# Optimization experiments

Hardware: AMD Instinct MI355X
Metric: run time of the kernel (lower is better)

## Reference

```python
import jax, jax.numpy as jnp
import numpy as np

B, NODES, D, DEG = 256, 124, 32, 16
N = B * NODES
EP = NODES * DEG
E = B * EP
L, H, C = 3, 4, 32
NCLS = 40
TMP = 124 + 32 * 2 * L
EPS = 1e-5
NEG_SLOPE = 0.2


def setup_inputs() -> dict:
    key = jax.random.key(0)
    ks = jax.random.split(key, 16)
    x = jax.random.normal(ks[0], (N, D), dtype=jnp.float32)
    # per-graph random edges, guaranteed no self-loops
    src = jax.random.randint(ks[1], (B, EP), 0, NODES)
    off = jax.random.randint(ks[2], (B, EP), 1, NODES)
    dst = (src + off) % NODES
    goff = (jnp.arange(B) * NODES)[:, None]
    edge_index = jnp.stack([(src + goff).reshape(-1), (dst + goff).reshape(-1)]).astype(jnp.int32)
    batch = jnp.repeat(jnp.arange(B), NODES).astype(jnp.int32)
    conv_W = jax.random.normal(ks[3], (L, D, H * C), dtype=jnp.float32) / np.sqrt(D)
    conv_att_l = jax.random.normal(ks[4], (L, H, C), dtype=jnp.float32) * 0.1
    conv_att_r = jax.random.normal(ks[5], (L, H, C), dtype=jnp.float32) * 0.1
    conv_bias = jnp.zeros((L, C), dtype=jnp.float32)
    bn_gamma = jnp.ones((L, C), dtype=jnp.float32)
    bn_beta = jnp.zeros((L, C), dtype=jnp.float32)
    lin1_W = jax.random.normal(ks[6], (NODES * C, 124), dtype=jnp.float32) / np.sqrt(NODES * C)
    lin1_b = jnp.zeros((124,), dtype=jnp.float32)
    bn1_gamma = jnp.ones((124,), dtype=jnp.float32)
    bn1_beta = jnp.zeros((124,), dtype=jnp.float32)
    lin2_W = jax.random.normal(ks[7], (TMP, NCLS), dtype=jnp.float32) / np.sqrt(TMP)
    lin2_b = jnp.zeros((NCLS,), dtype=jnp.float32)
    return dict(x=x, edge_index=edge_index, batch=batch, conv_W=conv_W,
                conv_att_l=conv_att_l, conv_att_r=conv_att_r, conv_bias=conv_bias,
                bn_gamma=bn_gamma, bn_beta=bn_beta, lin1_W=lin1_W, lin1_b=lin1_b,
                bn1_gamma=bn1_gamma, bn1_beta=bn1_beta, lin2_W=lin2_W, lin2_b=lin2_b)


def _supergat_mx(x, src, dst, W, att_l, att_r, bias):
    # SuperGATConv, attention_type='MX', concat=False (mean over heads), eval mode
    h = (x @ W).reshape(N, H, C)              # [N,H,C]
    x_j = h[src]                              # source / message features [E',H,C]
    x_i = h[dst]                              # target features
    logits = jnp.sum(x_i * x_j, -1)           # [E',H] dot-product logits
    alpha = jnp.sum(x_j * att_l, -1) + jnp.sum(x_i * att_r, -1)
    alpha = alpha * jax.nn.sigmoid(logits)
    alpha = jax.nn.leaky_relu(alpha, NEG_SLOPE)
    # scatter-softmax over incoming edges of each target node
    amax = jax.ops.segment_max(alpha, dst, num_segments=N)
    ex = jnp.exp(alpha - amax[dst])
    denom = jax.ops.segment_sum(ex, dst, num_segments=N)
    a = ex / (denom[dst] + 1e-16)             # [E',H]
    out = jax.ops.segment_sum(x_j * a[..., None], dst, num_segments=N)  # [N,H,C]
    return out.mean(axis=1) + bias            # concat=False -> head mean, [N,C]


def _batchnorm(x, gamma, beta):
    mu = x.mean(0)
    var = x.var(0)
    return (x - mu) * jax.lax.rsqrt(var + EPS) * gamma + beta


def reference(x, edge_index, batch, conv_W, conv_att_l, conv_att_r, conv_bias,
              bn_gamma, bn_beta, lin1_W, lin1_b, bn1_gamma, bn1_beta, lin2_W, lin2_b):
    # add self loops once (input edges contain none)
    sl = jnp.arange(N, dtype=edge_index.dtype)
    src = jnp.concatenate([edge_index[0], sl])
    dst = jnp.concatenate([edge_index[1], sl])
    inter = []
    for l in range(L):
        x = _supergat_mx(x, src, dst, conv_W[l], conv_att_l[l], conv_att_r[l], conv_bias[l])
        x = _batchnorm(x, bn_gamma[l], bn_beta[l])
        x = jax.nn.relu(x)
        cnt = jax.ops.segment_sum(jnp.ones((N,), x.dtype), batch, num_segments=B)
        gmean = jax.ops.segment_sum(x, batch, num_segments=B) / cnt[:, None]
        gmax = jax.ops.segment_max(x, batch, num_segments=B)
        inter.append(jnp.concatenate([gmean, gmax], 1))   # [B, 2C]
    x = x.reshape(B, NODES * C)
    x = x @ lin1_W + lin1_b
    x = _batchnorm(x, bn1_gamma, bn1_beta)
    x = jnp.concatenate([x] + inter, 1)                   # inter_connect=True
    x = jax.nn.relu(x)
    return x @ lin2_W + lin2_b                            # [B, NCLS]
```

## Files before the change

### kernel.cpp

```cpp
#include <hip/hip_runtime.h>
#include <math.h>

#define NN 31744
#define NE 507904
#define EP 1984
#define NODES 124
#define NB 256
#define CC 32
#define HC 128
#define FEAT_DIM 316
#define NCLS 40
#define NC 3968
#define EXCAP 192

typedef __attribute__((ext_vector_type(8))) short bf16x8;
typedef __attribute__((ext_vector_type(4))) float f32x4;

#define LOG2E  1.44269504f
#define LOG2E5 0.28853901f

__device__ __forceinline__ unsigned short f2bf(float f) {
    unsigned u = __float_as_uint(f);
    u = u + 0x7FFFu + ((u >> 16) & 1u);
    return (unsigned short)(u >> 16);
}
__device__ __forceinline__ float bf2f(unsigned short s) {
    return __uint_as_float(((unsigned)s) << 16);
}

__global__ __launch_bounds__(256) void mask_build(const int* __restrict__ ei,
                                                  unsigned* __restrict__ gmask,
                                                  int* __restrict__ gdst,
                                                  int* __restrict__ gdent,
                                                  float* __restrict__ bnacc) {
    __shared__ unsigned mcnt[NODES * NODES];
    __shared__ int cnt[128], pref[128];
    __shared__ int locs[124][8];
    int g = blockIdx.x, t = threadIdx.x;
    if (g == 0 && t < 192) bnacc[t] = 0.f;
    for (int i = t; i < NODES * NODES; i += 256) mcnt[i] = 0u;
    __syncthreads();
    for (int e = t; e < EP; e += 256) {
        int s = ei[g * EP + e] - g * NODES;
        int d = ei[NE + g * EP + e] - g * NODES;
        atomicAdd(&mcnt[d * NODES + s], 1u);
    }
    __syncthreads();
    int nd = 0;
    if (t < 124) {
        unsigned m[4] = {0u, 0u, 0u, 0u};
        for (int s = 0; s < NODES; ++s) {
            unsigned c = mcnt[t * NODES + s] + (s == t ? 1u : 0u);
            if (c) {
                m[s >> 5] |= 1u << (s & 31);
                if (c > 1u && nd < 8) { locs[t][nd] = (s << 8) | (int)c; nd++; }
            }
        }
        uint4 mm; mm.x = m[0]; mm.y = m[1]; mm.z = m[2]; mm.w = m[3];
        *(uint4*)&gmask[(size_t)(g * NODES + t) * 4] = mm;
        cnt[t] = nd;
    } else if (t < 128) cnt[t] = 0;
    __syncthreads();
    if (t < 128) pref[t] = cnt[t];
    __syncthreads();
    for (int off = 1; off < 128; off <<= 1) {
        int v = (t >= off && t < 128) ? pref[t - off] : 0;
        __syncthreads();
        if (t < 128) pref[t] += v;
        __syncthreads();
    }
    if (t < 124) {
        int off = pref[t] - cnt[t];
        gdst[g * 132 + t] = off < EXCAP ? off : EXCAP;
        for (int j = 0; j < nd; ++j)
            if (off + j < EXCAP) gdent[g * EXCAP + off + j] = locs[t][j];
    }
    if (t == 0) {
        int tot = pref[127];
        gdst[g * 132 + 124] = tot < EXCAP ? tot : EXCAP;
    }
}

__global__ __launch_bounds__(256) void wtrans(const float* __restrict__ W,
                                              unsigned short* __restrict__ WT) {
    __shared__ float tile[32][33];
    int kb = blockIdx.x, jb = blockIdx.y;
    int t = threadIdx.x;
    int tr = t >> 5, tc = t & 31;
    for (int r = tr; r < 32; r += 8) {
        int k = kb * 32 + r, j = jb * 32 + tc;
        tile[r][tc] = (j < 124) ? W[k * 124 + j] : 0.f;
    }
    __syncthreads();
    for (int r = tr; r < 32; r += 8) {
        int j = jb * 32 + r, k = kb * 32 + tc;
        WT[(size_t)j * NC + k] = f2bf(tile[tc][r]);
    }
}

#define HS 136
#define TS 136
#define XS 40
#define ABS 136
#define PWS 40

__global__ __launch_bounds__(1024, 1) void conv_graph(
    const float* __restrict__ xin, const float* __restrict__ W,
    const float* __restrict__ attl, const float* __restrict__ attr,
    const float* __restrict__ bias,
    const unsigned* __restrict__ gmask, const int* __restrict__ gdst,
    const int* __restrict__ gdent,
    const float* __restrict__ bnprev, const float* __restrict__ gprev,
    const float* __restrict__ bprev, float* __restrict__ feat, int lprev,
    float* __restrict__ y, float* __restrict__ bnacc) {

    __shared__ short hbh[128 * HS];
    __shared__ short hbl[128 * HS];
    __shared__ short hTall[128 * TS];
    __shared__ short pwbuf[16 * 1280];
    __shared__ short attBuf[16 * ABS];
    __shared__ float ALs[4][128], ARs[4][128];
    __shared__ unsigned mask[128][4];
    __shared__ unsigned short dupst[136];
    __shared__ unsigned dupent[EXCAP];
    __shared__ float bias_s[32];
    __shared__ float bsum[8][32], bsq[8][32];
    __shared__ float pmean[32];
    __shared__ int pmax[32];

    int g = blockIdx.x, t = threadIdx.x, base = g * NODES;
    short* xh  = pwbuf;
    short* xl  = pwbuf + 5120;
    short* WTh = hTall;
    short* WTl = hTall + 5120;

    if (t < 32) { pmean[t] = 0.f; pmax[t] = 0; }
    __syncthreads();

    {
        const float4* xsrc = (const float4*)(xin + (size_t)base * CC);
        for (int i = t; i < 992; i += 1024) {
            float4 v = xsrc[i];
            int n = i >> 3, c4 = i & 7;
            if (lprev >= 0) {
                float vv[4] = {v.x, v.y, v.z, v.w};
#pragma unroll
                for (int q = 0; q < 4; ++q) {
                    int c = c4 * 4 + q;
                    float mu = bnprev[c] * (1.f / NN);
                    float var = bnprev[32 + c] * (1.f / NN) - mu * mu;
                    float sc = rsqrtf(var + 1e-5f) * gprev[c];
                    float xv = (vv[q] - mu) * sc + bprev[c];
                    xv = fmaxf(xv, 0.f);
                    vv[q] = xv;
                    atomicAdd(&pmean[c], xv);
                    atomicMax(&pmax[c], __float_as_int(xv));
                }
                v.x = vv[0]; v.y = vv[1]; v.z = vv[2]; v.w = vv[3];
            }
            unsigned short h0 = f2bf(v.x), h1 = f2bf(v.y), h2 = f2bf(v.z), h3 = f2bf(v.w);
            unsigned short l0 = f2bf(v.x - bf2f(h0)), l1 = f2bf(v.y - bf2f(h1));
            unsigned short l2 = f2bf(v.z - bf2f(h2)), l3 = f2bf(v.w - bf2f(h3));
            uint2 ph; ph.x = ((unsigned)h1 << 16) | h0; ph.y = ((unsigned)h3 << 16) | h2;
            uint2 pl; pl.x = ((unsigned)l1 << 16) | l0; pl.y = ((unsigned)l3 << 16) | l2;
            *(uint2*)&xh[n * XS + c4 * 4] = ph;
            *(uint2*)&xl[n * XS + c4 * 4] = pl;
        }
        if (t < 4 * XS) { xh[124 * XS + t] = 0; xl[124 * XS + t] = 0; }
    }
    {
        int hc = t & 127, mq = t >> 7, ks = mq * 4;
        unsigned short hh4[4], ll4[4];
#pragma unroll
        for (int q = 0; q < 4; ++q) {
            float w = W[(ks + q) * HC + hc];
            hh4[q] = f2bf(w);
            ll4[q] = f2bf(w - bf2f(hh4[q]));
        }
        uint2 ph; ph.x = ((unsigned)hh4[1] << 16) | hh4[0]; ph.y = ((unsigned)hh4[3] << 16) | hh4[2];
        uint2 pl; pl.x = ((unsigned)ll4[1] << 16) | ll4[0]; pl.y = ((unsigned)ll4[3] << 16) | ll4[2];
        *(uint2*)&WTh[hc * XS + ks] = ph;
        *(uint2*)&WTl[hc * XS + ks] = pl;
    }
    for (int i = t; i < 2048; i += 1024) {
        int n = i >> 7, k = i & 127;
        float v = 0.f;
        int hidx = n & 3;
        if (n < 8 && (k >> 5) == hidx)
            v = (n < 4) ? attl[hidx * 32 + (k & 31)] : attr[hidx * 32 + (k & 31)];
        attBuf[n * ABS + k] = (short)f2bf(v);
    }
    if (t < CC) bias_s[t] = bias[t];
    if (t < 128) {
        if (t < 124) {
            uint4 m = *(const uint4*)&gmask[(size_t)(base + t) * 4];
            mask[t][0] = m.x; mask[t][1] = m.y; mask[t][2] = m.z; mask[t][3] = m.w;
        } else { mask[t][0] = 0u; mask[t][1] = 0u; mask[t][2] = 0u; mask[t][3] = 0u; }
    }
    if (t < 136) dupst[t] = (unsigned short)gdst[g * 132 + (t < 124 ? t : 124)];
    if (t >= 832 && t < 832 + EXCAP) dupent[t - 832] = (unsigned)gdent[g * EXCAP + (t - 832)];
    __syncthreads();

    if (lprev >= 0 && t < 32) {
        float* fp = feat + g * FEAT_DIM + NODES + lprev * 64;
        fp[t] = pmean[t] * (1.f / NODES);
        fp[32 + t] = __int_as_float(pmax[t]);
    }

    int wv = t >> 6, l = t & 63;
    int l15 = l & 15, l4 = l >> 4;

#pragma unroll
    for (int j = 0; j < 4; ++j) {
        int idx = wv * 4 + j;
        int tr = idx >> 3, tc = idx & 7;
        bf16x8 ah = *(bf16x8*)&xh[(tr * 16 + l15) * XS + l4 * 8];
        bf16x8 al_ = *(bf16x8*)&xl[(tr * 16 + l15) * XS + l4 * 8];
        bf16x8 bh = *(bf16x8*)&WTh[(tc * 16 + l15) * XS + l4 * 8];
        bf16x8 bl_ = *(bf16x8*)&WTl[(tc * 16 + l15) * XS + l4 * 8];
        f32x4 z = {0.f, 0.f, 0.f, 0.f};
        f32x4 c0 = __builtin_amdgcn_mfma_f32_16x16x32_bf16(ah, bh, z, 0, 0, 0);
        f32x4 c1 = __builtin_amdgcn_mfma_f32_16x16x32_bf16(ah, bl_, z, 0, 0, 0);
        f32x4 c2 = __builtin_amdgcn_mfma_f32_16x16x32_bf16(al_, bh, z, 0, 0, 0);
        f32x4 c = (c0 + c1) + c2;
        int hc = tc * 16 + l15;
#pragma unroll
        for (int r = 0; r < 4; ++r) {
            int n = tr * 16 + l4 * 4 + r;
            float s = c[r];
            unsigned short hi = f2bf(s);
            hbh[n * HS + hc] = (short)hi;
            hbl[n * HS + hc] = (short)f2bf(s - bf2f(hi));
        }
    }
    __syncthreads();

    if (wv < 8) {
        f32x4 c = {0.f, 0.f, 0.f, 0.f};
#pragma unroll
        for (int kb = 0; kb < 4; ++kb) {
            bf16x8 a = *(bf16x8*)&hbh[(wv * 16 + l15) * HS + kb * 32 + l4 * 8];
            bf16x8 b = *(bf16x8*)&attBuf[l15 * ABS + kb * 32 + l4 * 8];
            c = __builtin_amdgcn_mfma_f32_16x16x32_bf16(a, b, c, 0, 0, 0);
        }
        if (l15 < 8) {
#pragma unroll
            for (int r = 0; r < 4; ++r) {
                int n = wv * 16 + l4 * 4 + r;
                if (l15 < 4) ALs[l15][n] = c[r];
                else         ARs[l15 - 4][n] = c[r];
            }
        }
    }
#pragma unroll
    for (int hh2 = 0; hh2 < 4; ++hh2) {
        int k = t & 31, n4 = t >> 5;
        unsigned short r4[4];
#pragma unroll
        for (int r = 0; r < 4; ++r)
            r4[r] = (unsigned short)hbh[(n4 * 4 + r) * HS + hh2 * 32 + k];
        uint2 pk;
        pk.x = ((unsigned)r4[1] << 16) | r4[0];
        pk.y = ((unsigned)r4[3] << 16) | r4[2];
        *(uint2*)&hTall[(hh2 * 32 + k) * TS + n4 * 4] = pk;
    }
    __syncthreads();

    int DJ = wv >> 1;
    float accA[4] = {0.f, 0.f, 0.f, 0.f};
    float accB[4] = {0.f, 0.f, 0.f, 0.f};
    {
        int hh0 = (wv & 1) * 2;
        short* pwb = pwbuf + wv * 1280;
        int dst = DJ * 16 + l15;
        uint4 mrow = *(uint4*)&mask[dst][0];
        unsigned mwords[4] = {mrow.x, mrow.y, mrow.z, mrow.w};
        unsigned cntp[8];
#pragma unroll
        for (int SI = 0; SI < 8; ++SI) {
            unsigned mw = (mwords[SI >> 1] >> ((SI & 1) * 16 + l4 * 4)) & 0xFu;
            cntp[SI] = (mw & 1u) | ((mw & 2u) << 7) | ((mw & 4u) << 14) | ((mw & 8u) << 21);
        }
        {
            int s0 = dupst[dst], s1 = dupst[dst + 1];
            for (int e = s0; e < s1; ++e) {
                unsigned ent = dupent[e];
                unsigned src = (ent >> 8) & 255u;
                unsigned SI = src >> 4;
                unsigned r = (src & 15u) - (unsigned)(l4 * 4);
                if (r < 4u) {
                    unsigned sh = 8u * r;
                    cntp[SI] = (cntp[SI] & ~(255u << sh)) | ((ent & 255u) << sh);
                }
            }
        }

#define GRAM(kb, slot) { \
    _Pragma("unroll") \
    for (int s2 = 0; s2 < 2; ++s2) { \
        int SI = (kb) * 2 + s2; \
        int ao = (SI * 16 + l15) * HS + hh * 32 + l4 * 8; \
        bf16x8 ah = *(bf16x8*)&hbh[ao]; \
        bf16x8 al_ = *(bf16x8*)&hbl[ao]; \
        f32x4 z2 = {0.f, 0.f, 0.f, 0.f}; \
        f32x4 c0 = __builtin_amdgcn_mfma_f32_16x16x32_bf16(ah, gb, z2, 0, 0, 0); \
        f32x4 c1 = __builtin_amdgcn_mfma_f32_16x16x32_bf16(ah, gl, z2, 0, 0, 0); \
        f32x4 c2 = __builtin_amdgcn_mfma_f32_16x16x32_bf16(al_, gb, z2, 0, 0, 0); \
        f32x4 c = (c0 + c1) + c2; \
        int src0 = SI * 16 + l4 * 4; \
        float4 al4 = *(float4*)&ALs[hh][src0]; \
        unsigned cp = cntp[SI]; \
        float pv[4]; \
        _Pragma("unroll") \
        for (int r = 0; r < 4; ++r) { \
            float e2 = __builtin_amdgcn_exp2f(-LOG2E * c[r]); \
            float sig = __builtin_amdgcn_rcpf(1.f + e2); \
            float a2 = (((const float*)&al4)[r] + ar) * sig; \
            float m = fmaxf(a2 * LOG2E, a2 * LOG2E5); \
            float cr = (float)((cp >> (8 * r)) & 255u); \
            pv[r] = __builtin_amdgcn_exp2f(m) * cr; \
        } \
        sden += (pv[0] + pv[1]) + (pv[2] + pv[3]); \
        unsigned w0_, w1_; \
        asm("v_cvt_pk_bf16_f32 %0, %1, %2" : "=v"(w0_) : "v"(pv[0]), "v"(pv[1])); \
        asm("v_cvt_pk_bf16_f32 %0, %1, %2" : "=v"(w1_) : "v"(pv[2]), "v"(pv[3])); \
        uint2 pk_; pk_.x = w0_; pk_.y = w1_; \
        *(uint2*)&pwb[(slot) * 640 + l15 * PWS + s2 * 16 + l4 * 4] = pk_; \
    } }

#define PVOP(kb, slot) { \
    bf16x8 a = *(bf16x8*)&pwb[(slot) * 640 + l15 * PWS + l4 * 8]; \
    bf16x8 b0 = *(bf16x8*)&hTall[(hh * 32 + l15) * TS + (kb) * 32 + l4 * 8]; \
    bf16x8 b1 = *(bf16x8*)&hTall[(hh * 32 + 16 + l15) * TS + (kb) * 32 + l4 * 8]; \
    num0 = __builtin_amdgcn_mfma_f32_16x16x32_bf16(a, b0, num0, 0, 0, 0); \
    num1 = __builtin_amdgcn_mfma_f32_16x16x32_bf16(a, b1, num1, 0, 0, 0); }

#pragma unroll
        for (int jj = 0; jj < 2; ++jj) {
            int hh = hh0 + jj;
            bf16x8 gb = *(bf16x8*)&hbh[dst * HS + hh * 32 + l4 * 8];
            bf16x8 gl = *(bf16x8*)&hbl[dst * HS + hh * 32 + l4 * 8];
            float ar = ARs[hh][dst];
            float sden = 0.f;
            f32x4 num0 = {0.f, 0.f, 0.f, 0.f};
            f32x4 num1 = {0.f, 0.f, 0.f, 0.f};
            GRAM(0, 0);
            GRAM(1, 1); PVOP(0, 0);
            GRAM(2, 0); PVOP(1, 1);
            GRAM(3, 1); PVOP(2, 0);
            PVOP(3, 1);
            sden += __shfl_xor(sden, 16, 64);
            sden += __shfl_xor(sden, 32, 64);
#pragma unroll
            for (int r = 0; r < 4; ++r) {
                float dn = __shfl(sden, l4 * 4 + r, 64) + 1e-16f;
                accA[r] += ((float*)&num0)[r] / dn;
                accB[r] += ((float*)&num1)[r] / dn;
            }
        }
#undef GRAM
#undef PVOP
    }
    __syncthreads();

    float* exch = (float*)pwbuf;
    if (wv & 1) {
#pragma unroll
        for (int r = 0; r < 4; ++r) {
            exch[DJ * 512 + l15 * 16 + l4 * 4 + r] = accA[r];
            exch[DJ * 512 + 256 + l15 * 16 + l4 * 4 + r] = accB[r];
        }
    }
    __syncthreads();

    if (!(wv & 1)) {
        float sA = 0.f, qA = 0.f, sB = 0.f, qB = 0.f;
#pragma unroll
        for (int r = 0; r < 4; ++r) {
            int n = DJ * 16 + l4 * 4 + r;
            float a = accA[r] + exch[DJ * 512 + l15 * 16 + l4 * 4 + r];
            float b = accB[r] + exch[DJ * 512 + 256 + l15 * 16 + l4 * 4 + r];
            a = 0.25f * a + bias_s[l15];
            b = 0.25f * b + bias_s[16 + l15];
            if (n < NODES) {
                y[(size_t)(base + n) * CC + l15] = a;
                y[(size_t)(base + n) * CC + 16 + l15] = b;
                sA += a; qA += a * a; sB += b; qB += b * b;
            }
        }
        sA += __shfl_xor(sA, 16, 64); sA += __shfl_xor(sA, 32, 64);
        qA += __shfl_xor(qA, 16, 64); qA += __shfl_xor(qA, 32, 64);
        sB += __shfl_xor(sB, 16, 64); sB += __shfl_xor(sB, 32, 64);
        qB += __shfl_xor(qB, 16, 64); qB += __shfl_xor(qB, 32, 64);
        if (l < 16) {
            bsum[DJ][l15] = sA; bsum[DJ][16 + l15] = sB;
            bsq[DJ][l15] = qA;  bsq[DJ][16 + l15] = qB;
        }
    }
    __syncthreads();
    if (t < CC) {
        float S = 0.f, Q = 0.f;
#pragma unroll
        for (int w = 0; w < 8; ++w) { S += bsum[w][t]; Q += bsq[w][t]; }
        atomicAdd(&bnacc[t], S);
        atomicAdd(&bnacc[CC + t], Q);
    }
}

__global__ void bn_relu_pool(const float* __restrict__ y, const float* __restrict__ acc,
                             const float* __restrict__ gamma, const float* __restrict__ beta,
                             unsigned short* __restrict__ xbf, float* __restrict__ feat, int l) {
    int g = blockIdx.x;
    int t = threadIdx.x;
    int c = t & 31, r0 = t >> 5;
    float mu = acc[c] * (1.f / NN);
    float var = acc[32 + c] * (1.f / NN) - mu * mu;
    float sc = rsqrtf(var + 1e-5f) * gamma[c];
    float bt = beta[c];
    float s = 0.f, mx = -INFINITY;
    for (int r = r0; r < NODES; r += 4) {
        int i = (g * NODES + r) * CC + c;
        float v = (y[i] - mu) * sc + bt;
        v = fmaxf(v, 0.f);
        xbf[i] = f2bf(v);
        s += v; mx = fmaxf(mx, v);
    }
    __shared__ float ls[128], lm[128];
    ls[t] = s; lm[t] = mx;
    __syncthreads();
    if (t < 32) {
        float S = ls[t] + ls[32 + t] + ls[64 + t] + ls[96 + t];
        float M = fmaxf(fmaxf(lm[t], lm[32 + t]), fmaxf(lm[64 + t], lm[96 + t]));
        float* fp = feat + g * FEAT_DIM + NODES + l * 64;
        fp[t] = S * (1.f / NODES);
        fp[32 + t] = M;
    }
}

#define L1_KS 4
#define L1_KC 992
#define XP 1000
__global__ __launch_bounds__(512) void lin1_mfma(const unsigned short* __restrict__ Xb,
                                                 const unsigned short* __restrict__ WT,
                                                 float* __restrict__ part) {
    __shared__ unsigned short Xs[16 * XP];
    int mt = blockIdx.x >> 2, kp = blockIdx.x & 3;
    int t = threadIdx.x;
    int wv = t >> 6, l = t & 63, l15 = l & 15, l4 = l >> 4;
    int M0 = mt * 16, k0 = kp * L1_KC;
    for (int i = t; i < 16 * 124; i += 512) {
        int r = i / 124, c = i - r * 124;
        *(uint4*)&Xs[r * XP + c * 8] = *(const uint4*)&Xb[(size_t)(M0 + r) * NC + k0 + c * 8];
    }
    __syncthreads();
    int N0 = wv * 16;
    f32x4 acc = {0.f, 0.f, 0.f, 0.f};
#pragma unroll 4
    for (int kk = 0; kk < 31; ++kk) {
        bf16x8 a = *(bf16x8*)&Xs[l15 * XP + kk * 32 + l4 * 8];
        bf16x8 b = *(const bf16x8*)&WT[(size_t)(N0 + l15) * NC + k0 + kk * 32 + l4 * 8];
        acc = __builtin_amdgcn_mfma_f32_16x16x32_bf16(a, b, acc, 0, 0, 0);
    }
    if (N0 + l15 < 124) {
#pragma unroll
        for (int r = 0; r < 4; ++r)
            part[(size_t)kp * NB * 124 + (M0 + l4 * 4 + r) * 124 + N0 + l15] = acc[r];
    }
}

__global__ void lin1_reduce(const float* __restrict__ part, const float* __restrict__ b,
                            float* __restrict__ out1) {
    int i = blockIdx.x * blockDim.x + threadIdx.x;
    if (i >= NB * 124) return;
    int j = i % 124;
    float s = b[j];
#pragma unroll
    for (int ks = 0; ks < L1_KS; ++ks) s += part[ks * NB * 124 + i];
    out1[i] = s;
}

__global__ void bn1_relu(const float* __restrict__ out1, const float* __restrict__ gamma,
                         const float* __restrict__ beta, float* __restrict__ feat) {
    __shared__ float ps[4][124], pq[4][124], smu[124], ssc[124], sbt[124];
    int t = threadIdx.x;
    int c = t & 127, seg = t >> 7;
    float s = 0.f, q = 0.f;
    if (c < 124) {
        for (int b = seg * 64; b < seg * 64 + 64; ++b) {
            float v = out1[b * 124 + c]; s += v; q += v * v;
        }
        ps[seg][c] = s; pq[seg][c] = q;
    }
    __syncthreads();
    if (t < 124) {
        float S = ps[0][t] + ps[1][t] + ps[2][t] + ps[3][t];
        float Q = pq[0][t] + pq[1][t] + pq[2][t] + pq[3][t];
        float mu = S * (1.f / NB);
        float var = Q * (1.f / NB) - mu * mu;
        smu[t] = mu; ssc[t] = rsqrtf(var + 1e-5f) * gamma[t]; sbt[t] = beta[t];
    }
    __syncthreads();
    if (c < 124) {
        for (int b = seg * 64; b < seg * 64 + 64; ++b) {
            float v = (out1[b * 124 + c] - smu[c]) * ssc[c] + sbt[c];
            feat[b * FEAT_DIM + c] = fmaxf(v, 0.f);
        }
    }
}

__global__ void lin2_k(const float* __restrict__ feat, const float* __restrict__ W,
                       const float* __restrict__ b, float* __restrict__ out) {
    __shared__ float psum[8][40];
    int g = blockIdx.x;
    int t = threadIdx.x;
    int j = t % 40, u = t / 40;
    if (u < 8) {
        int k0 = u * 40, k1 = (u == 7) ? FEAT_DIM : k0 + 40;
        float s = 0.f;
        for (int k = k0; k < k1; ++k) s += feat[g * FEAT_DIM + k] * W[k * NCLS + j];
        psum[u][j] = s;
    }
    __syncthreads();
    if (t < NCLS) {
        float s = b[t];
#pragma unroll
        for (int u2 = 0; u2 < 8; ++u2) s += psum[u2][t];
        out[g * NCLS + t] = s;
    }
}

extern "C" void kernel_launch(void* const* d_in, const int* in_sizes, int n_in,
                              void* d_out, int out_size, void* d_ws, size_t ws_size,
                              hipStream_t stream) {
    const float* x      = (const float*)d_in[0];
    const int*   ei     = (const int*)d_in[1];
    const float* conv_W = (const float*)d_in[3];
    const float* att_l  = (const float*)d_in[4];
    const float* att_r  = (const float*)d_in[5];
    const float* conv_b = (const float*)d_in[6];
    const float* bn_g   = (const float*)d_in[7];
    const float* bn_b   = (const float*)d_in[8];
    const float* lin1_W = (const float*)d_in[9];
    const float* lin1_b = (const float*)d_in[10];
    const float* bn1_g  = (const float*)d_in[11];
    const float* bn1_b  = (const float*)d_in[12];
    const float* lin2_W = (const float*)d_in[13];
    const float* lin2_b = (const float*)d_in[14];

    float* ws = (float*)d_ws;
    float* y = ws;
    unsigned short* xbf = (unsigned short*)(y + (size_t)NN * CC);
    float* bnacc = (float*)(xbf + (size_t)NN * CC);
    float* feat  = bnacc + 192;
    float* out1  = feat + NB * FEAT_DIM;
    float* part  = out1 + NB * 124;
    unsigned short* WT = (unsigned short*)(part + L1_KS * NB * 124);
    unsigned* gmask = (unsigned*)(WT + (size_t)128 * NC);
    int* gdst  = (int*)(gmask + (size_t)NN * 4);
    int* gdent = gdst + NB * 132;

    mask_build<<<NB, 256, 0, stream>>>(ei, gmask, gdst, gdent, bnacc);
    wtrans<<<dim3(NC / 32, 4), 256, 0, stream>>>(lin1_W, WT);

    const float* xin = x;
    for (int l = 0; l < 3; ++l) {
        const float* bnprev = (l == 0) ? nullptr : bnacc + (l - 1) * 64;
        const float* gprev  = (l == 0) ? bn_g : bn_g + (l - 1) * CC;
        const float* bprev  = (l == 0) ? bn_b : bn_b + (l - 1) * CC;
        conv_graph<<<NB, 1024, 0, stream>>>(xin, conv_W + l * CC * HC,
                                            att_l + l * HC, att_r + l * HC,
                                            conv_b + l * CC, gmask, gdst, gdent,
                                            bnprev, gprev, bprev, feat, l - 1,
                                            y, bnacc + l * 64);
        xin = y;
    }

    bn_relu_pool<<<NB, 128, 0, stream>>>(y, bnacc + 128, bn_g + 2 * CC, bn_b + 2 * CC,
                                         xbf, feat, 2);
    lin1_mfma<<<64, 512, 0, stream>>>(xbf, WT, part);
    lin1_reduce<<<(NB * 124 + 255) / 256, 256, 0, stream>>>(part, lin1_b, out1);
    bn1_relu<<<1, 512, 0, stream>>>(out1, bn1_g, bn1_b, feat);
    lin2_k<<<NB, 320, 0, stream>>>(feat, lin2_W, lin2_b, (float*)d_out);
}
```

Before: 145.6 us.

## Fuse mask build, three conv layers and BN pooling into one cooperative kernel

```diff
diff --git a/kernel.cpp b/kernel.cpp
--- a/kernel.cpp
+++ b/kernel.cpp
@@ -1,5 +1,8 @@
 #include <hip/hip_runtime.h>
+#include <hip/hip_cooperative_groups.h>
 #include <math.h>
+
+namespace cg = cooperative_groups;
 
 #define NN 31744
 #define NE 507904
@@ -28,64 +31,13 @@
     return __uint_as_float(((unsigned)s) << 16);
 }
 
-__global__ __launch_bounds__(256) void mask_build(const int* __restrict__ ei,
-                                                  unsigned* __restrict__ gmask,
-                                                  int* __restrict__ gdst,
-                                                  int* __restrict__ gdent,
-                                                  float* __restrict__ bnacc) {
-    __shared__ unsigned mcnt[NODES * NODES];
-    __shared__ int cnt[128], pref[128];
-    __shared__ int locs[124][8];
-    int g = blockIdx.x, t = threadIdx.x;
-    if (g == 0 && t < 192) bnacc[t] = 0.f;
-    for (int i = t; i < NODES * NODES; i += 256) mcnt[i] = 0u;
-    __syncthreads();
-    for (int e = t; e < EP; e += 256) {
-        int s = ei[g * EP + e] - g * NODES;
-        int d = ei[NE + g * EP + e] - g * NODES;
-        atomicAdd(&mcnt[d * NODES + s], 1u);
-    }
-    __syncthreads();
-    int nd = 0;
-    if (t < 124) {
-        unsigned m[4] = {0u, 0u, 0u, 0u};
-        for (int s = 0; s < NODES; ++s) {
-            unsigned c = mcnt[t * NODES + s] + (s == t ? 1u : 0u);
-            if (c) {
-                m[s >> 5] |= 1u << (s & 31);
-                if (c > 1u && nd < 8) { locs[t][nd] = (s << 8) | (int)c; nd++; }
-            }
-        }
-        uint4 mm; mm.x = m[0]; mm.y = m[1]; mm.z = m[2]; mm.w = m[3];
-        *(uint4*)&gmask[(size_t)(g * NODES + t) * 4] = mm;
-        cnt[t] = nd;
-    } else if (t < 128) cnt[t] = 0;
-    __syncthreads();
-    if (t < 128) pref[t] = cnt[t];
-    __syncthreads();
-    for (int off = 1; off < 128; off <<= 1) {
-        int v = (t >= off && t < 128) ? pref[t - off] : 0;
-        __syncthreads();
-        if (t < 128) pref[t] += v;
-        __syncthreads();
-    }
-    if (t < 124) {
-        int off = pref[t] - cnt[t];
-        gdst[g * 132 + t] = off < EXCAP ? off : EXCAP;
-        for (int j = 0; j < nd; ++j)
-            if (off + j < EXCAP) gdent[g * EXCAP + off + j] = locs[t][j];
-    }
-    if (t == 0) {
-        int tot = pref[127];
-        gdst[g * 132 + 124] = tot < EXCAP ? tot : EXCAP;
-    }
-}
-
 __global__ __launch_bounds__(256) void wtrans(const float* __restrict__ W,
-                                              unsigned short* __restrict__ WT) {
+                                              unsigned short* __restrict__ WT,
+                                              float* __restrict__ bnacc) {
     __shared__ float tile[32][33];
     int kb = blockIdx.x, jb = blockIdx.y;
     int t = threadIdx.x;
+    if (kb == 0 && jb == 0 && t < 192) bnacc[t] = 0.f;
     int tr = t >> 5, tc = t & 31;
     for (int r = tr; r < 32; r += 8) {
         int k = kb * 32 + r, j = jb * 32 + tc;
@@ -104,18 +56,15 @@
 #define ABS 136
 #define PWS 40
 
-__global__ __launch_bounds__(1024, 1) void conv_graph(
-    const float* __restrict__ xin, const float* __restrict__ W,
+__global__ __launch_bounds__(1024, 1) void conv3(
+    const float* __restrict__ x, const float* __restrict__ Wall,
     const float* __restrict__ attl, const float* __restrict__ attr,
-    const float* __restrict__ bias,
-    const unsigned* __restrict__ gmask, const int* __restrict__ gdst,
-    const int* __restrict__ gdent,
-    const float* __restrict__ bnprev, const float* __restrict__ gprev,
-    const float* __restrict__ bprev, float* __restrict__ feat, int lprev,
-    float* __restrict__ y, float* __restrict__ bnacc) {
-
-    __shared__ short hbh[128 * HS];
-    __shared__ short hbl[128 * HS];
+    const float* __restrict__ ball, const float* __restrict__ bng,
+    const float* __restrict__ bnb, const int* __restrict__ ei,
+    unsigned short* __restrict__ xbf, float* __restrict__ feat,
+    float* __restrict__ bnacc) {
+
+    __shared__ short hpool[2 * 128 * HS];
     __shared__ short hTall[128 * TS];
     __shared__ short pwbuf[16 * 1280];
     __shared__ short attBuf[16 * ABS];
@@ -125,175 +74,196 @@
     __shared__ unsigned dupent[EXCAP];
     __shared__ float bias_s[32];
     __shared__ float bsum[8][32], bsq[8][32];
-    __shared__ float pmean[32];
-    __shared__ int pmax[32];
-
-    int g = blockIdx.x, t = threadIdx.x, base = g * NODES;
+    __shared__ int cnt_s[128], pref_s[128];
+
+    short* hbh = hpool;
+    short* hbl = hpool + 128 * HS;
     short* xh  = pwbuf;
     short* xl  = pwbuf + 5120;
     short* WTh = hTall;
     short* WTl = hTall + 5120;
 
-    if (t < 32) { pmean[t] = 0.f; pmax[t] = 0; }
-    __syncthreads();
+    cg::grid_group grid = cg::this_grid();
+    int g = blockIdx.x, t = threadIdx.x, base = g * NODES;
+    int wv = t >> 6, l = t & 63;
+    int l15 = l & 15, l4 = l >> 4;
+    int DJ = wv >> 1;
 
     {
-        const float4* xsrc = (const float4*)(xin + (size_t)base * CC);
-        for (int i = t; i < 992; i += 1024) {
-            float4 v = xsrc[i];
-            int n = i >> 3, c4 = i & 7;
-            if (lprev >= 0) {
-                float vv[4] = {v.x, v.y, v.z, v.w};
-#pragma unroll
-                for (int q = 0; q < 4; ++q) {
-                    int c = c4 * 4 + q;
-                    float mu = bnprev[c] * (1.f / NN);
-                    float var = bnprev[32 + c] * (1.f / NN) - mu * mu;
-                    float sc = rsqrtf(var + 1e-5f) * gprev[c];
-                    float xv = (vv[q] - mu) * sc + bprev[c];
-                    xv = fmaxf(xv, 0.f);
-                    vv[q] = xv;
-                    atomicAdd(&pmean[c], xv);
-                    atomicMax(&pmax[c], __float_as_int(xv));
-                }
-                v.x = vv[0]; v.y = vv[1]; v.z = vv[2]; v.w = vv[3];
-            }
+        const float4* xsrc = (const float4*)(x + (size_t)base * CC);
+        if (t < 992) {
+            float4 v = xsrc[t];
+            int n = t >> 3, c4 = t & 7;
             unsigned short h0 = f2bf(v.x), h1 = f2bf(v.y), h2 = f2bf(v.z), h3 = f2bf(v.w);
-            unsigned short l0 = f2bf(v.x - bf2f(h0)), l1 = f2bf(v.y - bf2f(h1));
-            unsigned short l2 = f2bf(v.z - bf2f(h2)), l3 = f2bf(v.w - bf2f(h3));
+            unsigned short q0 = f2bf(v.x - bf2f(h0)), q1 = f2bf(v.y - bf2f(h1));
+            unsigned short q2 = f2bf(v.z - bf2f(h2)), q3 = f2bf(v.w - bf2f(h3));
             uint2 ph; ph.x = ((unsigned)h1 << 16) | h0; ph.y = ((unsigned)h3 << 16) | h2;
-            uint2 pl; pl.x = ((unsigned)l1 << 16) | l0; pl.y = ((unsigned)l3 << 16) | l2;
+            uint2 pl; pl.x = ((unsigned)q1 << 16) | q0; pl.y = ((unsigned)q3 << 16) | q2;
             *(uint2*)&xh[n * XS + c4 * 4] = ph;
             *(uint2*)&xl[n * XS + c4 * 4] = pl;
         }
         if (t < 4 * XS) { xh[124 * XS + t] = 0; xl[124 * XS + t] = 0; }
     }
+
     {
-        int hc = t & 127, mq = t >> 7, ks = mq * 4;
-        unsigned short hh4[4], ll4[4];
-#pragma unroll
-        for (int q = 0; q < 4; ++q) {
-            float w = W[(ks + q) * HC + hc];
-            hh4[q] = f2bf(w);
-            ll4[q] = f2bf(w - bf2f(hh4[q]));
-        }
-        uint2 ph; ph.x = ((unsigned)hh4[1] << 16) | hh4[0]; ph.y = ((unsigned)hh4[3] << 16) | hh4[2];
-        uint2 pl; pl.x = ((unsigned)ll4[1] << 16) | ll4[0]; pl.y = ((unsigned)ll4[3] << 16) | ll4[2];
-        *(uint2*)&WTh[hc * XS + ks] = ph;
-        *(uint2*)&WTl[hc * XS + ks] = pl;
-    }
-    for (int i = t; i < 2048; i += 1024) {
-        int n = i >> 7, k = i & 127;
-        float v = 0.f;
-        int hidx = n & 3;
-        if (n < 8 && (k >> 5) == hidx)
-            v = (n < 4) ? attl[hidx * 32 + (k & 31)] : attr[hidx * 32 + (k & 31)];
-        attBuf[n * ABS + k] = (short)f2bf(v);
-    }
-    if (t < CC) bias_s[t] = bias[t];
-    if (t < 128) {
+        unsigned* mcnt = (unsigned*)hpool;
+        int (*locs)[8] = (int(*)[8])hTall;
+        for (int i = t; i < NODES * NODES; i += 1024) mcnt[i] = 0u;
+        __syncthreads();
+        for (int e = t; e < EP; e += 1024) {
+            int s = ei[g * EP + e] - base;
+            int d = ei[NE + g * EP + e] - base;
+            atomicAdd(&mcnt[d * NODES + s], 1u);
+        }
+        __syncthreads();
+        int nd = 0;
         if (t < 124) {
-            uint4 m = *(const uint4*)&gmask[(size_t)(base + t) * 4];
-            mask[t][0] = m.x; mask[t][1] = m.y; mask[t][2] = m.z; mask[t][3] = m.w;
-        } else { mask[t][0] = 0u; mask[t][1] = 0u; mask[t][2] = 0u; mask[t][3] = 0u; }
-    }
-    if (t < 136) dupst[t] = (unsigned short)gdst[g * 132 + (t < 124 ? t : 124)];
-    if (t >= 832 && t < 832 + EXCAP) dupent[t - 832] = (unsigned)gdent[g * EXCAP + (t - 832)];
-    __syncthreads();
-
-    if (lprev >= 0 && t < 32) {
-        float* fp = feat + g * FEAT_DIM + NODES + lprev * 64;
-        fp[t] = pmean[t] * (1.f / NODES);
-        fp[32 + t] = __int_as_float(pmax[t]);
-    }
-
-    int wv = t >> 6, l = t & 63;
-    int l15 = l & 15, l4 = l >> 4;
-
-#pragma unroll
-    for (int j = 0; j < 4; ++j) {
-        int idx = wv * 4 + j;
-        int tr = idx >> 3, tc = idx & 7;
-        bf16x8 ah = *(bf16x8*)&xh[(tr * 16 + l15) * XS + l4 * 8];
-        bf16x8 al_ = *(bf16x8*)&xl[(tr * 16 + l15) * XS + l4 * 8];
-        bf16x8 bh = *(bf16x8*)&WTh[(tc * 16 + l15) * XS + l4 * 8];
-        bf16x8 bl_ = *(bf16x8*)&WTl[(tc * 16 + l15) * XS + l4 * 8];
-        f32x4 z = {0.f, 0.f, 0.f, 0.f};
-        f32x4 c0 = __builtin_amdgcn_mfma_f32_16x16x32_bf16(ah, bh, z, 0, 0, 0);
-        f32x4 c1 = __builtin_amdgcn_mfma_f32_16x16x32_bf16(ah, bl_, z, 0, 0, 0);
-        f32x4 c2 = __builtin_amdgcn_mfma_f32_16x16x32_bf16(al_, bh, z, 0, 0, 0);
-        f32x4 c = (c0 + c1) + c2;
-        int hc = tc * 16 + l15;
-#pragma unroll
-        for (int r = 0; r < 4; ++r) {
-            int n = tr * 16 + l4 * 4 + r;
-            float s = c[r];
-            unsigned short hi = f2bf(s);
-            hbh[n * HS + hc] = (short)hi;
-            hbl[n * HS + hc] = (short)f2bf(s - bf2f(hi));
-        }
-    }
-    __syncthreads();
-
-    if (wv < 8) {
-        f32x4 c = {0.f, 0.f, 0.f, 0.f};
-#pragma unroll
-        for (int kb = 0; kb < 4; ++kb) {
-            bf16x8 a = *(bf16x8*)&hbh[(wv * 16 + l15) * HS + kb * 32 + l4 * 8];
-            bf16x8 b = *(bf16x8*)&attBuf[l15 * ABS + kb * 32 + l4 * 8];
-            c = __builtin_amdgcn_mfma_f32_16x16x32_bf16(a, b, c, 0, 0, 0);
-        }
-        if (l15 < 8) {
+            unsigned m[4] = {0u, 0u, 0u, 0u};
+            for (int s = 0; s < NODES; ++s) {
+                unsigned c = mcnt[t * NODES + s] + (s == t ? 1u : 0u);
+                if (c) {
+                    m[s >> 5] |= 1u << (s & 31);
+                    if (c > 1u && nd < 8) { locs[t][nd] = (s << 8) | (int)c; nd++; }
+                }
+            }
+            mask[t][0] = m[0]; mask[t][1] = m[1]; mask[t][2] = m[2]; mask[t][3] = m[3];
+            cnt_s[t] = nd;
+        } else if (t < 128) {
+            cnt_s[t] = 0;
+            mask[t][0] = 0u; mask[t][1] = 0u; mask[t][2] = 0u; mask[t][3] = 0u;
+        }
+        __syncthreads();
+        if (t < 128) pref_s[t] = cnt_s[t];
+        __syncthreads();
+        for (int off = 1; off < 128; off <<= 1) {
+            int v = (t >= off && t < 128) ? pref_s[t - off] : 0;
+            __syncthreads();
+            if (t < 128) pref_s[t] += v;
+            __syncthreads();
+        }
+        if (t < 124) {
+            int off = pref_s[t] - cnt_s[t];
+            dupst[t] = (unsigned short)(off < EXCAP ? off : EXCAP);
+            for (int j = 0; j < nd; ++j)
+                if (off + j < EXCAP) dupent[off + j] = (unsigned)locs[t][j];
+        } else if (t < 136) {
+            int tot = pref_s[127];
+            dupst[t] = (unsigned short)(tot < EXCAP ? tot : EXCAP);
+        }
+        __syncthreads();
+    }
+
+    for (int lyr = 0; lyr < 3; ++lyr) {
+        const float* W = Wall + lyr * CC * HC;
+        {
+            int hc = t & 127, mq = t >> 7, ks = mq * 4;
+            unsigned short hh4[4], ll4[4];
+#pragma unroll
+            for (int q = 0; q < 4; ++q) {
+                float w = W[(ks + q) * HC + hc];
+                hh4[q] = f2bf(w);
+                ll4[q] = f2bf(w - bf2f(hh4[q]));
+            }
+            uint2 ph; ph.x = ((unsigned)hh4[1] << 16) | hh4[0]; ph.y = ((unsigned)hh4[3] << 16) | hh4[2];
+            uint2 pl; pl.x = ((unsigned)ll4[1] << 16) | ll4[0]; pl.y = ((unsigned)ll4[3] << 16) | ll4[2];
+            *(uint2*)&WTh[hc * XS + ks] = ph;
+            *(uint2*)&WTl[hc * XS + ks] = pl;
+        }
+        for (int i = t; i < 2048; i += 1024) {
+            int n = i >> 7, k = i & 127;
+            float v = 0.f;
+            int hidx = n & 3;
+            if (n < 8 && (k >> 5) == hidx)
+                v = (n < 4) ? attl[lyr * HC + hidx * 32 + (k & 31)]
+                            : attr[lyr * HC + hidx * 32 + (k & 31)];
+            attBuf[n * ABS + k] = (short)f2bf(v);
+        }
+        if (t < CC) bias_s[t] = ball[lyr * CC + t];
+        __syncthreads();
+
+#pragma unroll
+        for (int j = 0; j < 4; ++j) {
+            int idx = wv * 4 + j;
+            int tr = idx >> 3, tc = idx & 7;
+            bf16x8 ah = *(bf16x8*)&xh[(tr * 16 + l15) * XS + l4 * 8];
+            bf16x8 al_ = *(bf16x8*)&xl[(tr * 16 + l15) * XS + l4 * 8];
+            bf16x8 bh = *(bf16x8*)&WTh[(tc * 16 + l15) * XS + l4 * 8];
+            bf16x8 bl_ = *(bf16x8*)&WTl[(tc * 16 + l15) * XS + l4 * 8];
+            f32x4 z = {0.f, 0.f, 0.f, 0.f};
+            f32x4 c0 = __builtin_amdgcn_mfma_f32_16x16x32_bf16(ah, bh, z, 0, 0, 0);
+            f32x4 c1 = __builtin_amdgcn_mfma_f32_16x16x32_bf16(ah, bl_, z, 0, 0, 0);
+            f32x4 c2 = __builtin_amdgcn_mfma_f32_16x16x32_bf16(al_, bh, z, 0, 0, 0);
+            f32x4 c = (c0 + c1) + c2;
+            int hc = tc * 16 + l15;
 #pragma unroll
             for (int r = 0; r < 4; ++r) {
-                int n = wv * 16 + l4 * 4 + r;
-                if (l15 < 4) ALs[l15][n] = c[r];
-                else         ARs[l15 - 4][n] = c[r];
-            }
-        }
-    }
-#pragma unroll
-    for (int hh2 = 0; hh2 < 4; ++hh2) {
-        int k = t & 31, n4 = t >> 5;
-        unsigned short r4[4];
-#pragma unroll
-        for (int r = 0; r < 4; ++r)
-            r4[r] = (unsigned short)hbh[(n4 * 4 + r) * HS + hh2 * 32 + k];
-        uint2 pk;
-        pk.x = ((unsigned)r4[1] << 16) | r4[0];
-        pk.y = ((unsigned)r4[3] << 16) | r4[2];
-        *(uint2*)&hTall[(hh2 * 32 + k) * TS + n4 * 4] = pk;
-    }
-    __syncthreads();
-
-    int DJ = wv >> 1;
-    float accA[4] = {0.f, 0.f, 0.f, 0.f};
-    float accB[4] = {0.f, 0.f, 0.f, 0.f};
-    {
-        int hh0 = (wv & 1) * 2;
-        short* pwb = pwbuf + wv * 1280;
-        int dst = DJ * 16 + l15;
-        uint4 mrow = *(uint4*)&mask[dst][0];
-        unsigned mwords[4] = {mrow.x, mrow.y, mrow.z, mrow.w};
-        unsigned cntp[8];
-#pragma unroll
-        for (int SI = 0; SI < 8; ++SI) {
-            unsigned mw = (mwords[SI >> 1] >> ((SI & 1) * 16 + l4 * 4)) & 0xFu;
-            cntp[SI] = (mw & 1u) | ((mw & 2u) << 7) | ((mw & 4u) << 14) | ((mw & 8u) << 21);
-        }
+                int n = tr * 16 + l4 * 4 + r;
+                float s = c[r];
+                unsigned short hi = f2bf(s);
+                hbh[n * HS + hc] = (short)hi;
+                hbl[n * HS + hc] = (short)f2bf(s - bf2f(hi));
+            }
+        }
+        __syncthreads();
+
+        if (wv < 8) {
+            f32x4 c = {0.f, 0.f, 0.f, 0.f};
+#pragma unroll
+            for (int kb = 0; kb < 4; ++kb) {
+                bf16x8 a = *(bf16x8*)&hbh[(wv * 16 + l15) * HS + kb * 32 + l4 * 8];
+                bf16x8 b = *(bf16x8*)&attBuf[l15 * ABS + kb * 32 + l4 * 8];
+                c = __builtin_amdgcn_mfma_f32_16x16x32_bf16(a, b, c, 0, 0, 0);
+            }
+            if (l15 < 8) {
+#pragma unroll
+                for (int r = 0; r < 4; ++r) {
+                    int n = wv * 16 + l4 * 4 + r;
+                    if (l15 < 4) ALs[l15][n] = c[r];
+                    else         ARs[l15 - 4][n] = c[r];
+                }
+            }
+        }
+#pragma unroll
+        for (int hh2 = 0; hh2 < 4; ++hh2) {
+            int k = t & 31, n4 = t >> 5;
+            unsigned short r4[4];
+#pragma unroll
+            for (int r = 0; r < 4; ++r)
+                r4[r] = (unsigned short)hbh[(n4 * 4 + r) * HS + hh2 * 32 + k];
+            uint2 pk;
+            pk.x = ((unsigned)r4[1] << 16) | r4[0];
+            pk.y = ((unsigned)r4[3] << 16) | r4[2];
+            *(uint2*)&hTall[(hh2 * 32 + k) * TS + n4 * 4] = pk;
+        }
+        __syncthreads();
+
+        float accA[4] = {0.f, 0.f, 0.f, 0.f};
+        float accB[4] = {0.f, 0.f, 0.f, 0.f};
         {
-            int s0 = dupst[dst], s1 = dupst[dst + 1];
-            for (int e = s0; e < s1; ++e) {
-                unsigned ent = dupent[e];
-                unsigned src = (ent >> 8) & 255u;
-                unsigned SI = src >> 4;
-                unsigned r = (src & 15u) - (unsigned)(l4 * 4);
-                if (r < 4u) {
-                    unsigned sh = 8u * r;
-                    cntp[SI] = (cntp[SI] & ~(255u << sh)) | ((ent & 255u) << sh);
+            int hh0 = (wv & 1) * 2;
+            short* pwb = pwbuf + wv * 1280;
+            int dst = DJ * 16 + l15;
+            uint4 mrow = *(uint4*)&mask[dst][0];
+            unsigned mwords[4] = {mrow.x, mrow.y, mrow.z, mrow.w};
+            unsigned cntp[8];
+#pragma unroll
+            for (int SI = 0; SI < 8; ++SI) {
+                unsigned mw = (mwords[SI >> 1] >> ((SI & 1) * 16 + l4 * 4)) & 0xFu;
+                cntp[SI] = (mw & 1u) | ((mw & 2u) << 7) | ((mw & 4u) << 14) | ((mw & 8u) << 21);
+            }
+            {
+                int s0 = dupst[dst], s1 = dupst[dst + 1];
+                for (int e = s0; e < s1; ++e) {
+                    unsigned ent = dupent[e];
+                    unsigned src = (ent >> 8) & 255u;
+                    unsigned SI = src >> 4;
+                    unsigned r = (src & 15u) - (unsigned)(l4 * 4);
+                    if (r < 4u) {
+                        unsigned sh = 8u * r;
+                        cntp[SI] = (cntp[SI] & ~(255u << sh)) | ((ent & 255u) << sh);
+                    }
                 }
             }
-        }
 
 #define GRAM(kb, slot) { \
     _Pragma("unroll") \
@@ -336,104 +306,126 @@
     num1 = __builtin_amdgcn_mfma_f32_16x16x32_bf16(a, b1, num1, 0, 0, 0); }
 
 #pragma unroll
-        for (int jj = 0; jj < 2; ++jj) {
-            int hh = hh0 + jj;
-            bf16x8 gb = *(bf16x8*)&hbh[dst * HS + hh * 32 + l4 * 8];
-            bf16x8 gl = *(bf16x8*)&hbl[dst * HS + hh * 32 + l4 * 8];
-            float ar = ARs[hh][dst];
-            float sden = 0.f;
-            f32x4 num0 = {0.f, 0.f, 0.f, 0.f};
-            f32x4 num1 = {0.f, 0.f, 0.f, 0.f};
-            GRAM(0, 0);
-            GRAM(1, 1); PVOP(0, 0);
-            GRAM(2, 0); PVOP(1, 1);
-            GRAM(3, 1); PVOP(2, 0);
-            PVOP(3, 1);
-            sden += __shfl_xor(sden, 16, 64);
-            sden += __shfl_xor(sden, 32, 64);
-#pragma unroll
-            for (int r = 0; r < 4; ++r) {
-                float dn = __shfl(sden, l4 * 4 + r, 64) + 1e-16f;
-                accA[r] += ((float*)&num0)[r] / dn;
-                accB[r] += ((float*)&num1)[r] / dn;
-            }
-        }
+            for (int jj = 0; jj < 2; ++jj) {
+                int hh = hh0 + jj;
+                bf16x8 gb = *(bf16x8*)&hbh[dst * HS + hh * 32 + l4 * 8];
+                bf16x8 gl = *(bf16x8*)&hbl[dst * HS + hh * 32 + l4 * 8];
+                float ar = ARs[hh][dst];
+                float sden = 0.f;
+                f32x4 num0 = {0.f, 0.f, 0.f, 0.f};
+                f32x4 num1 = {0.f, 0.f, 0.f, 0.f};
+                GRAM(0, 0);
+                GRAM(1, 1); PVOP(0, 0);
+                GRAM(2, 0); PVOP(1, 1);
+                GRAM(3, 1); PVOP(2, 0);
+                PVOP(3, 1);
+                sden += __shfl_xor(sden, 16, 64);
+                sden += __shfl_xor(sden, 32, 64);
+#pragma unroll
+                for (int r = 0; r < 4; ++r) {
+                    float dn = __shfl(sden, l4 * 4 + r, 64) + 1e-16f;
+                    accA[r] += ((float*)&num0)[r] / dn;
+                    accB[r] += ((float*)&num1)[r] / dn;
+                }
+            }
 #undef GRAM
 #undef PVOP
-    }
-    __syncthreads();
-
-    float* exch = (float*)pwbuf;
-    if (wv & 1) {
-#pragma unroll
-        for (int r = 0; r < 4; ++r) {
-            exch[DJ * 512 + l15 * 16 + l4 * 4 + r] = accA[r];
-            exch[DJ * 512 + 256 + l15 * 16 + l4 * 4 + r] = accB[r];
-        }
-    }
-    __syncthreads();
-
-    if (!(wv & 1)) {
-        float sA = 0.f, qA = 0.f, sB = 0.f, qB = 0.f;
-#pragma unroll
-        for (int r = 0; r < 4; ++r) {
-            int n = DJ * 16 + l4 * 4 + r;
-            float a = accA[r] + exch[DJ * 512 + l15 * 16 + l4 * 4 + r];
-            float b = accB[r] + exch[DJ * 512 + 256 + l15 * 16 + l4 * 4 + r];
-            a = 0.25f * a + bias_s[l15];
-            b = 0.25f * b + bias_s[16 + l15];
-            if (n < NODES) {
-                y[(size_t)(base + n) * CC + l15] = a;
-                y[(size_t)(base + n) * CC + 16 + l15] = b;
-                sA += a; qA += a * a; sB += b; qB += b * b;
-            }
-        }
-        sA += __shfl_xor(sA, 16, 64); sA += __shfl_xor(sA, 32, 64);
-        qA += __shfl_xor(qA, 16, 64); qA += __shfl_xor(qA, 32, 64);
-        sB += __shfl_xor(sB, 16, 64); sB += __shfl_xor(sB, 32, 64);
-        qB += __shfl_xor(qB, 16, 64); qB += __shfl_xor(qB, 32, 64);
-        if (l < 16) {
-            bsum[DJ][l15] = sA; bsum[DJ][16 + l15] = sB;
-            bsq[DJ][l15] = qA;  bsq[DJ][16 + l15] = qB;
-        }
-    }
-    __syncthreads();
-    if (t < CC) {
-        float S = 0.f, Q = 0.f;
-#pragma unroll
-        for (int w = 0; w < 8; ++w) { S += bsum[w][t]; Q += bsq[w][t]; }
-        atomicAdd(&bnacc[t], S);
-        atomicAdd(&bnacc[CC + t], Q);
-    }
-}
-
-__global__ void bn_relu_pool(const float* __restrict__ y, const float* __restrict__ acc,
-                             const float* __restrict__ gamma, const float* __restrict__ beta,
-                             unsigned short* __restrict__ xbf, float* __restrict__ feat, int l) {
-    int g = blockIdx.x;
-    int t = threadIdx.x;
-    int c = t & 31, r0 = t >> 5;
-    float mu = acc[c] * (1.f / NN);
-    float var = acc[32 + c] * (1.f / NN) - mu * mu;
-    float sc = rsqrtf(var + 1e-5f) * gamma[c];
-    float bt = beta[c];
-    float s = 0.f, mx = -INFINITY;
-    for (int r = r0; r < NODES; r += 4) {
-        int i = (g * NODES + r) * CC + c;
-        float v = (y[i] - mu) * sc + bt;
-        v = fmaxf(v, 0.f);
-        xbf[i] = f2bf(v);
-        s += v; mx = fmaxf(mx, v);
-    }
-    __shared__ float ls[128], lm[128];
-    ls[t] = s; lm[t] = mx;
-    __syncthreads();
-    if (t < 32) {
-        float S = ls[t] + ls[32 + t] + ls[64 + t] + ls[96 + t];
-        float M = fmaxf(fmaxf(lm[t], lm[32 + t]), fmaxf(lm[64 + t], lm[96 + t]));
-        float* fp = feat + g * FEAT_DIM + NODES + l * 64;
-        fp[t] = S * (1.f / NODES);
-        fp[32 + t] = M;
+        }
+        __syncthreads();
+
+        float* exch = (float*)pwbuf;
+        if (wv & 1) {
+#pragma unroll
+            for (int r = 0; r < 4; ++r) {
+                exch[DJ * 512 + l15 * 16 + l4 * 4 + r] = accA[r];
+                exch[DJ * 512 + 256 + l15 * 16 + l4 * 4 + r] = accB[r];
+            }
+        }
+        __syncthreads();
+
+        float va[4] = {0.f, 0.f, 0.f, 0.f};
+        float vb[4] = {0.f, 0.f, 0.f, 0.f};
+        if (!(wv & 1)) {
+            float sA = 0.f, qA = 0.f, sB = 0.f, qB = 0.f;
+#pragma unroll
+            for (int r = 0; r < 4; ++r) {
+                int n = DJ * 16 + l4 * 4 + r;
+                float a = accA[r] + exch[DJ * 512 + l15 * 16 + l4 * 4 + r];
+                float b = accB[r] + exch[DJ * 512 + 256 + l15 * 16 + l4 * 4 + r];
+                a = 0.25f * a + bias_s[l15];
+                b = 0.25f * b + bias_s[16 + l15];
+                va[r] = a; vb[r] = b;
+                if (n < NODES) { sA += a; qA += a * a; sB += b; qB += b * b; }
+            }
+            sA += __shfl_xor(sA, 16, 64); sA += __shfl_xor(sA, 32, 64);
+            qA += __shfl_xor(qA, 16, 64); qA += __shfl_xor(qA, 32, 64);
+            sB += __shfl_xor(sB, 16, 64); sB += __shfl_xor(sB, 32, 64);
+            qB += __shfl_xor(qB, 16, 64); qB += __shfl_xor(qB, 32, 64);
+            if (l < 16) {
+                bsum[DJ][l15] = sA; bsum[DJ][16 + l15] = sB;
+                bsq[DJ][l15] = qA;  bsq[DJ][16 + l15] = qB;
+            }
+        }
+        __syncthreads();
+        if (t < CC) {
+            float S = 0.f, Q = 0.f;
+#pragma unroll
+            for (int w = 0; w < 8; ++w) { S += bsum[w][t]; Q += bsq[w][t]; }
+            atomicAdd(&bnacc[lyr * 64 + t], S);
+            atomicAdd(&bnacc[lyr * 64 + CC + t], Q);
+        }
+        grid.sync();
+
+        if (!(wv & 1)) {
+            float muA = bnacc[lyr * 64 + l15] * (1.f / NN);
+            float vrA = bnacc[lyr * 64 + 32 + l15] * (1.f / NN) - muA * muA;
+            float scA = rsqrtf(vrA + 1e-5f) * bng[lyr * CC + l15];
+            float btA = bnb[lyr * CC + l15];
+            float muB = bnacc[lyr * 64 + 16 + l15] * (1.f / NN);
+            float vrB = bnacc[lyr * 64 + 48 + l15] * (1.f / NN) - muB * muB;
+            float scB = rsqrtf(vrB + 1e-5f) * bng[lyr * CC + 16 + l15];
+            float btB = bnb[lyr * CC + 16 + l15];
+            float sA = 0.f, mA = -INFINITY, sB = 0.f, mB = -INFINITY;
+#pragma unroll
+            for (int r = 0; r < 4; ++r) {
+                int n = DJ * 16 + l4 * 4 + r;
+                float a = fmaxf((va[r] - muA) * scA + btA, 0.f);
+                float b = fmaxf((vb[r] - muB) * scB + btB, 0.f);
+                if (n < NODES) {
+                    sA += a; mA = fmaxf(mA, a); sB += b; mB = fmaxf(mB, b);
+                    if (lyr < 2) {
+                        unsigned short ha = f2bf(a);
+                        xh[n * XS + l15] = (short)ha;
+                        xl[n * XS + l15] = (short)f2bf(a - bf2f(ha));
+                        unsigned short hb = f2bf(b);
+                        xh[n * XS + 16 + l15] = (short)hb;
+                        xl[n * XS + 16 + l15] = (short)f2bf(b - bf2f(hb));
+                    } else {
+                        xbf[(size_t)(base + n) * CC + l15] = f2bf(a);
+                        xbf[(size_t)(base + n) * CC + 16 + l15] = f2bf(b);
+                    }
+                }
+            }
+            sA += __shfl_xor(sA, 16, 64); sA += __shfl_xor(sA, 32, 64);
+            sB += __shfl_xor(sB, 16, 64); sB += __shfl_xor(sB, 32, 64);
+            mA = fmaxf(mA, __shfl_xor(mA, 16, 64)); mA = fmaxf(mA, __shfl_xor(mA, 32, 64));
+            mB = fmaxf(mB, __shfl_xor(mB, 16, 64)); mB = fmaxf(mB, __shfl_xor(mB, 32, 64));
+            if (l < 16) {
+                bsum[DJ][l15] = sA; bsum[DJ][16 + l15] = sB;
+                bsq[DJ][l15] = mA;  bsq[DJ][16 + l15] = mB;
+            }
+        }
+        if (lyr < 2 && t < 4 * XS) { xh[124 * XS + t] = 0; xl[124 * XS + t] = 0; }
+        __syncthreads();
+        if (t < CC) {
+            float S = 0.f, M = -INFINITY;
+#pragma unroll
+            for (int w = 0; w < 8; ++w) { S += bsum[w][t]; M = fmaxf(M, bsq[w][t]); }
+            float* fp = feat + g * FEAT_DIM + NODES + lyr * 64;
+            fp[t] = S * (1.f / NODES);
+            fp[32 + t] = M;
+        }
+        __syncthreads();
     }
 }
 
@@ -548,35 +540,20 @@
     const float* lin2_b = (const float*)d_in[14];
 
     float* ws = (float*)d_ws;
-    float* y = ws;
-    unsigned short* xbf = (unsigned short*)(y + (size_t)NN * CC);
+    unsigned short* xbf = (unsigned short*)ws;
     float* bnacc = (float*)(xbf + (size_t)NN * CC);
     float* feat  = bnacc + 192;
     float* out1  = feat + NB * FEAT_DIM;
     float* part  = out1 + NB * 124;
     unsigned short* WT = (unsigned short*)(part + L1_KS * NB * 124);
-    unsigned* gmask = (unsigned*)(WT + (size_t)128 * NC);
-    int* gdst  = (int*)(gmask + (size_t)NN * 4);
-    int* gdent = gdst + NB * 132;
-
-    mask_build<<<NB, 256, 0, stream>>>(ei, gmask, gdst, gdent, bnacc);
-    wtrans<<<dim3(NC / 32, 4), 256, 0, stream>>>(lin1_W, WT);
-
-    const float* xin = x;
-    for (int l = 0; l < 3; ++l) {
-        const float* bnprev = (l == 0) ? nullptr : bnacc + (l - 1) * 64;
-        const float* gprev  = (l == 0) ? bn_g : bn_g + (l - 1) * CC;
-        const float* bprev  = (l == 0) ? bn_b : bn_b + (l - 1) * CC;
-        conv_graph<<<NB, 1024, 0, stream>>>(xin, conv_W + l * CC * HC,
-                                            att_l + l * HC, att_r + l * HC,
-                                            conv_b + l * CC, gmask, gdst, gdent,
-                                            bnprev, gprev, bprev, feat, l - 1,
-                                            y, bnacc + l * 64);
-        xin = y;
-    }
-
-    bn_relu_pool<<<NB, 128, 0, stream>>>(y, bnacc + 128, bn_g + 2 * CC, bn_b + 2 * CC,
-                                         xbf, feat, 2);
+
+    wtrans<<<dim3(NC / 32, 4), 256, 0, stream>>>(lin1_W, WT, bnacc);
+
+    void* cargs[] = {(void*)&x, (void*)&conv_W, (void*)&att_l, (void*)&att_r,
+                     (void*)&conv_b, (void*)&bn_g, (void*)&bn_b, (void*)&ei,
+                     (void*)&xbf, (void*)&feat, (void*)&bnacc};
+    hipLaunchCooperativeKernel((const void*)conv3, dim3(NB), dim3(1024), cargs, 0, stream);
+
     lin1_mfma<<<64, 512, 0, stream>>>(xbf, WT, part);
     lin1_reduce<<<(NB * 124 + 255) / 256, 256, 0, stream>>>(part, lin1_b, out1);
     bn1_relu<<<1, 512, 0, stream>>>(out1, bn1_g, bn1_b, feat);
```

Measured after the change: 221.7 us. 1.52x slower.
